# Kernel optimization log

Hardware: AMD Instinct MI355X
Metric: run time of the kernel (lower is better)

The kernel has to match this reference:

```python
import jax, jax.numpy as jnp
import numpy as np

EPS = 1e-08


def setup_inputs() -> dict:
    key = jax.random.key(0)
    B, C, T = 4, 512, 32000
    x = jax.random.normal(key, (B, C, T), dtype=jnp.float32)
    weight = jnp.ones((C,), dtype=jnp.float32)
    bias = jnp.zeros((C,), dtype=jnp.float32)
    return {"x": x, "weight": weight, "bias": bias}


def reference(x, weight, bias):
    # Cumulative LayerNorm over (C, 0..t) for each time step t, 3D input (B, C, T).
    # Note: sum_C(cumsum_T(x)) == cumsum_T(sum_C(x)); reduce channels first (cheaper, same math).
    B, C, T = x.shape
    step = jnp.arange(1, T + 1, dtype=x.dtype)            # (T,)
    count = (step * C)[None, None, :]                     # (1,1,T)
    cum_sum = jnp.cumsum(x.sum(axis=1, keepdims=True), axis=-1)          # (B,1,T)
    cum_sum_sq = jnp.cumsum((x * x).sum(axis=1, keepdims=True), axis=-1)  # (B,1,T)
    cum_mean = cum_sum / count
    cum_var = jnp.maximum(cum_sum_sq / count - cum_mean * cum_mean, 0.0)
    y = (x - cum_mean) / jnp.sqrt(cum_var + EPS)
    return y * weight[None, :, None] + bias[None, :, None]
```

## Files before the change

### kernel.cpp

```cpp
#include <hip/hip_runtime.h>
#include <math.h>

#define EPS 1e-8

constexpr int CSPLIT = 16;
constexpr int CH = 1024;

__global__ __launch_bounds__(256) void clnorm_colsum_b(
    const float4* __restrict__ x4, float4* __restrict__ psum4,
    float4* __restrict__ psumsq4, int b, int C, int T4) {
  int t4 = blockIdx.x * 256 + threadIdx.x;
  if (t4 >= T4) return;
  int s = blockIdx.y;
  int cPer = C / CSPLIT;
  const float4* xp = x4 + ((size_t)b * C + (size_t)s * cPer) * (size_t)T4 + t4;
  float4 sum = make_float4(0.f, 0.f, 0.f, 0.f);
  float4 sq = make_float4(0.f, 0.f, 0.f, 0.f);
#pragma unroll 8
  for (int c = 0; c < cPer; ++c) {
    float4 v = xp[(size_t)c * T4];
    sum.x += v.x;
    sum.y += v.y;
    sum.z += v.z;
    sum.w += v.w;
    sq.x = fmaf(v.x, v.x, sq.x);
    sq.y = fmaf(v.y, v.y, sq.y);
    sq.z = fmaf(v.z, v.z, sq.z);
    sq.w = fmaf(v.w, v.w, sq.w);
  }
  size_t o = (size_t)s * T4 + t4;
  psum4[o] = sum;
  psumsq4[o] = sq;
}

__global__ __launch_bounds__(256) void clnorm_chunktot_b(
    const float4* __restrict__ psum4, const float4* __restrict__ psumsq4,
    double* __restrict__ chunkTot, int T4) {
  int ch = blockIdx.x;
  int tid = threadIdx.x;
  int t4 = ch * 256 + tid;
  double ls = 0.0, lq = 0.0;
  if (t4 < T4) {
#pragma unroll
    for (int k = 0; k < CSPLIT; ++k) {
      float4 s4 = psum4[(size_t)k * T4 + t4];
      float4 q4 = psumsq4[(size_t)k * T4 + t4];
      ls += (double)((s4.x + s4.y) + (s4.z + s4.w));
      lq += (double)((q4.x + q4.y) + (q4.z + q4.w));
    }
  }
  __shared__ double sh_s[256];
  __shared__ double sh_q[256];
  sh_s[tid] = ls;
  sh_q[tid] = lq;
  __syncthreads();
  for (int off = 128; off > 0; off >>= 1) {
    if (tid < off) {
      sh_s[tid] += sh_s[tid + off];
      sh_q[tid] += sh_q[tid + off];
    }
    __syncthreads();
  }
  if (tid == 0) {
    chunkTot[(size_t)ch * 2 + 0] = sh_s[0];
    chunkTot[(size_t)ch * 2 + 1] = sh_q[0];
  }
}

__global__ __launch_bounds__(256) void clnorm_scanemit_b(
    const float4* __restrict__ psum4, const float4* __restrict__ psumsq4,
    const double* __restrict__ chunkTot, float* __restrict__ mean,
    float* __restrict__ rstd, int b, int C, int T, int nCh) {
  int ch = blockIdx.x;
  int tid = threadIdx.x;
  int T4 = T / 4;
  int t4 = ch * 256 + tid;

  __shared__ double tp_s[256];
  __shared__ double tp_q[256];
  __shared__ double off_sq[2];

  if (tid == 0) {
    double os = 0.0, oq = 0.0;
    for (int c0 = 0; c0 < ch; ++c0) {
      os += chunkTot[(size_t)c0 * 2 + 0];
      oq += chunkTot[(size_t)c0 * 2 + 1];
    }
    off_sq[0] = os;
    off_sq[1] = oq;
  }

  double ds[4] = {0.0, 0.0, 0.0, 0.0};
  double dq[4] = {0.0, 0.0, 0.0, 0.0};
  if (t4 < T4) {
#pragma unroll
    for (int k = 0; k < CSPLIT; ++k) {
      float4 s4 = psum4[(size_t)k * T4 + t4];
      float4 q4 = psumsq4[(size_t)k * T4 + t4];
      ds[0] += (double)s4.x;
      ds[1] += (double)s4.y;
      ds[2] += (double)s4.z;
      ds[3] += (double)s4.w;
      dq[0] += (double)q4.x;
      dq[1] += (double)q4.y;
      dq[2] += (double)q4.z;
      dq[3] += (double)q4.w;
    }
  }
  double ts = (ds[0] + ds[1]) + (ds[2] + ds[3]);
  double tq = (dq[0] + dq[1]) + (dq[2] + dq[3]);
  tp_s[tid] = ts;
  tp_q[tid] = tq;
  __syncthreads();
  for (int off = 1; off < 256; off <<= 1) {
    double vs = (tid >= off) ? tp_s[tid - off] : 0.0;
    double vq = (tid >= off) ? tp_q[tid - off] : 0.0;
    __syncthreads();
    tp_s[tid] += vs;
    tp_q[tid] += vq;
    __syncthreads();
  }
  double run_s = off_sq[0] + tp_s[tid] - ts;
  double run_q = off_sq[1] + tp_q[tid] - tq;

  int t0 = t4 * 4;
  float m_out[4], r_out[4];
#pragma unroll
  for (int j = 0; j < 4; ++j) {
    run_s += ds[j];
    run_q += dq[j];
    double cnt = (double)(t0 + j + 1) * (double)C;
    double m = run_s / cnt;
    double var = run_q / cnt - m * m;
    if (var < 0.0) var = 0.0;
    m_out[j] = (float)m;
    r_out[j] = (float)(1.0 / sqrt(var + EPS));
  }
  if (t0 < T) {
    size_t mo = (size_t)b * T + t0;
    *(float4*)(mean + mo) = make_float4(m_out[0], m_out[1], m_out[2], m_out[3]);
    *(float4*)(rstd + mo) = make_float4(r_out[0], r_out[1], r_out[2], r_out[3]);
  }
}

__global__ __launch_bounds__(256) void clnorm_apply_b(
    const float4* __restrict__ x4, const float* __restrict__ w,
    const float* __restrict__ bias, const float4* __restrict__ mean4,
    const float4* __restrict__ rstd4, float4* __restrict__ y4,
    int b, int C, int T4) {
  int t4 = blockIdx.x * 256 + threadIdx.x;
  if (t4 >= T4) return;
  int c = blockIdx.y;
  size_t id = ((size_t)b * C + c) * (size_t)T4 + t4;
  size_t mo = (size_t)b * T4 + t4;
  float4 xv = x4[id];
  float4 mv = mean4[mo];
  float4 rv = rstd4[mo];
  float wc = w[c];
  float bc = bias[c];
  float4 yv;
  yv.x = (xv.x - mv.x) * rv.x * wc + bc;
  yv.y = (xv.y - mv.y) * rv.y * wc + bc;
  yv.z = (xv.z - mv.z) * rv.z * wc + bc;
  yv.w = (xv.w - mv.w) * rv.w * wc + bc;
  y4[id] = yv;
}

extern "C" void kernel_launch(void* const* d_in, const int* in_sizes, int n_in,
                              void* d_out, int out_size, void* d_ws,
                              size_t ws_size, hipStream_t stream) {
  const float* x = (const float*)d_in[0];
  const float* w = (const float*)d_in[1];
  const float* bias = (const float*)d_in[2];
  float* out = (float*)d_out;

  const int B = 4;
  int C = in_sizes[1];
  int T = in_sizes[0] / (B * C);
  int T4 = T / 4;
  int nCh = (T + CH - 1) / CH;

  float* ws = (float*)d_ws;
  size_t pn = (size_t)CSPLIT * T;
  float* psum = ws;
  float* psumsq = psum + pn;
  float* mean = psumsq + pn;
  float* rstd = mean + (size_t)B * T;
  double* chunkTot = (double*)(rstd + (size_t)B * T);

  dim3 gc((T4 + 255) / 256, CSPLIT);
  dim3 g2(nCh);
  dim3 ga((T4 + 255) / 256, C);

  for (int b = 0; b < B; ++b) {
    clnorm_colsum_b<<<gc, 256, 0, stream>>>((const float4*)x, (float4*)psum,
                                            (float4*)psumsq, b, C, T4);
    clnorm_chunktot_b<<<g2, 256, 0, stream>>>((const float4*)psum,
                                              (const float4*)psumsq, chunkTot,
                                              T4);
    clnorm_scanemit_b<<<g2, 256, 0, stream>>>((const float4*)psum,
                                              (const float4*)psumsq, chunkTot,
                                              mean, rstd, b, C, T, nCh);
    clnorm_apply_b<<<ga, 256, 0, stream>>>((const float4*)x, w, bias,
                                           (const float4*)mean,
                                           (const float4*)rstd, (float4*)out,
                                           b, C, T4);
  }
}
```

Before: 529.9 us.

## Fuse cumulative layernorm into single-pass kernel with decoupled look-back scan

```diff
diff --git a/kernel.cpp b/kernel.cpp
--- a/kernel.cpp
+++ b/kernel.cpp
@@ -3,167 +3,207 @@
 
 #define EPS 1e-8
 
-constexpr int CSPLIT = 16;
-constexpr int CH = 1024;
-
-__global__ __launch_bounds__(256) void clnorm_colsum_b(
-    const float4* __restrict__ x4, float4* __restrict__ psum4,
-    float4* __restrict__ psumsq4, int b, int C, int T4) {
-  int t4 = blockIdx.x * 256 + threadIdx.x;
-  if (t4 >= T4) return;
-  int s = blockIdx.y;
-  int cPer = C / CSPLIT;
-  const float4* xp = x4 + ((size_t)b * C + (size_t)s * cPer) * (size_t)T4 + t4;
-  float4 sum = make_float4(0.f, 0.f, 0.f, 0.f);
-  float4 sq = make_float4(0.f, 0.f, 0.f, 0.f);
+constexpr int W = 32;
+constexpr int W4 = W / 4;
+constexpr int NTHR = 512;
+constexpr int PARTS = NTHR / W;
+constexpr int CMAX = 512;
+
+__device__ inline unsigned long long ld_acq(const unsigned long long* p) {
+  return __hip_atomic_load(p, __ATOMIC_ACQUIRE, __HIP_MEMORY_SCOPE_AGENT);
+}
+__device__ inline unsigned long long ld_rlx(const unsigned long long* p) {
+  return __hip_atomic_load(p, __ATOMIC_RELAXED, __HIP_MEMORY_SCOPE_AGENT);
+}
+__device__ inline void st_rlx(unsigned long long* p, unsigned long long v) {
+  __hip_atomic_store(p, v, __ATOMIC_RELAXED, __HIP_MEMORY_SCOPE_AGENT);
+}
+__device__ inline void st_rel(unsigned long long* p, unsigned long long v) {
+  __hip_atomic_store(p, v, __ATOMIC_RELEASE, __HIP_MEMORY_SCOPE_AGENT);
+}
+__device__ inline double u2d(unsigned long long u) {
+  return __builtin_bit_cast(double, u);
+}
+__device__ inline unsigned long long d2u(double d) {
+  return __builtin_bit_cast(unsigned long long, d);
+}
+
+__global__ __launch_bounds__(NTHR, 4) void clnorm_fused(
+    const float4* __restrict__ x4, const float* __restrict__ wgt,
+    const float* __restrict__ bias, float4* __restrict__ y4,
+    unsigned long long* __restrict__ ws_u64, int B, int C, int T, int nCh) {
+  const int T4 = T >> 2;
+  const int tid = threadIdx.x;
+
+  __shared__ float x_sh[CMAX * W];
+  __shared__ float ps_sh[PARTS * W];
+  __shared__ float pq_sh[PARTS * W];
+  __shared__ float w_sh[CMAX];
+  __shared__ float b_sh[CMAX];
+  __shared__ __align__(16) float m_sh[W];
+  __shared__ __align__(16) float r_sh[W];
+  __shared__ int sh_tile;
+
+  unsigned long long* counter = ws_u64;
+  unsigned long long* slots = ws_u64 + 8;
+
+  if (tid == 0)
+    sh_tile = (int)__hip_atomic_fetch_add(counter, 1ull, __ATOMIC_RELAXED,
+                                          __HIP_MEMORY_SCOPE_AGENT);
+  __syncthreads();
+  const int tile = sh_tile;
+  const int b = tile / nCh;
+  const int chunk = tile - b * nCh;
+  const int t0 = chunk * W;
+  const int t40 = t0 >> 2;
+
+  const int nF4 = C * W4;
+#pragma unroll 4
+  for (int f = tid; f < nF4; f += NTHR) {
+    int c = f >> 3;
+    int t4 = f & (W4 - 1);
+    float4 v = make_float4(0.f, 0.f, 0.f, 0.f);
+    if (t40 + t4 < T4) v = x4[(size_t)(b * C + c) * T4 + t40 + t4];
+    *(float4*)&x_sh[c * W + t4 * 4] = v;
+  }
+  for (int c = tid; c < C; c += NTHR) {
+    w_sh[c] = wgt[c];
+    b_sh[c] = bias[c];
+  }
+  __syncthreads();
+
+  {
+    int t = tid & (W - 1);
+    int part = tid >> 5;
+    int cPer = C / PARTS;
+    int c0 = part * cPer;
+    float s = 0.f, q = 0.f;
 #pragma unroll 8
-  for (int c = 0; c < cPer; ++c) {
-    float4 v = xp[(size_t)c * T4];
-    sum.x += v.x;
-    sum.y += v.y;
-    sum.z += v.z;
-    sum.w += v.w;
-    sq.x = fmaf(v.x, v.x, sq.x);
-    sq.y = fmaf(v.y, v.y, sq.y);
-    sq.z = fmaf(v.z, v.z, sq.z);
-    sq.w = fmaf(v.w, v.w, sq.w);
-  }
-  size_t o = (size_t)s * T4 + t4;
-  psum4[o] = sum;
-  psumsq4[o] = sq;
-}
-
-__global__ __launch_bounds__(256) void clnorm_chunktot_b(
-    const float4* __restrict__ psum4, const float4* __restrict__ psumsq4,
-    double* __restrict__ chunkTot, int T4) {
-  int ch = blockIdx.x;
-  int tid = threadIdx.x;
-  int t4 = ch * 256 + tid;
-  double ls = 0.0, lq = 0.0;
-  if (t4 < T4) {
+    for (int k = 0; k < cPer; ++k) {
+      float v = x_sh[(c0 + k) * W + t];
+      s += v;
+      q = fmaf(v, v, q);
+    }
+    ps_sh[part * W + t] = s;
+    pq_sh[part * W + t] = q;
+  }
+  __syncthreads();
+
+  if (tid < 64) {
+    const int lane = tid;
+    double p_s = 0.0, p_q = 0.0;
+    if (lane < W) {
 #pragma unroll
-    for (int k = 0; k < CSPLIT; ++k) {
-      float4 s4 = psum4[(size_t)k * T4 + t4];
-      float4 q4 = psumsq4[(size_t)k * T4 + t4];
-      ls += (double)((s4.x + s4.y) + (s4.z + s4.w));
-      lq += (double)((q4.x + q4.y) + (q4.z + q4.w));
-    }
-  }
-  __shared__ double sh_s[256];
-  __shared__ double sh_q[256];
-  sh_s[tid] = ls;
-  sh_q[tid] = lq;
-  __syncthreads();
-  for (int off = 128; off > 0; off >>= 1) {
-    if (tid < off) {
-      sh_s[tid] += sh_s[tid + off];
-      sh_q[tid] += sh_q[tid + off];
-    }
-    __syncthreads();
-  }
-  if (tid == 0) {
-    chunkTot[(size_t)ch * 2 + 0] = sh_s[0];
-    chunkTot[(size_t)ch * 2 + 1] = sh_q[0];
-  }
-}
-
-__global__ __launch_bounds__(256) void clnorm_scanemit_b(
-    const float4* __restrict__ psum4, const float4* __restrict__ psumsq4,
-    const double* __restrict__ chunkTot, float* __restrict__ mean,
-    float* __restrict__ rstd, int b, int C, int T, int nCh) {
-  int ch = blockIdx.x;
-  int tid = threadIdx.x;
-  int T4 = T / 4;
-  int t4 = ch * 256 + tid;
-
-  __shared__ double tp_s[256];
-  __shared__ double tp_q[256];
-  __shared__ double off_sq[2];
-
-  if (tid == 0) {
-    double os = 0.0, oq = 0.0;
-    for (int c0 = 0; c0 < ch; ++c0) {
-      os += chunkTot[(size_t)c0 * 2 + 0];
-      oq += chunkTot[(size_t)c0 * 2 + 1];
-    }
-    off_sq[0] = os;
-    off_sq[1] = oq;
-  }
-
-  double ds[4] = {0.0, 0.0, 0.0, 0.0};
-  double dq[4] = {0.0, 0.0, 0.0, 0.0};
-  if (t4 < T4) {
-#pragma unroll
-    for (int k = 0; k < CSPLIT; ++k) {
-      float4 s4 = psum4[(size_t)k * T4 + t4];
-      float4 q4 = psumsq4[(size_t)k * T4 + t4];
-      ds[0] += (double)s4.x;
-      ds[1] += (double)s4.y;
-      ds[2] += (double)s4.z;
-      ds[3] += (double)s4.w;
-      dq[0] += (double)q4.x;
-      dq[1] += (double)q4.y;
-      dq[2] += (double)q4.z;
-      dq[3] += (double)q4.w;
-    }
-  }
-  double ts = (ds[0] + ds[1]) + (ds[2] + ds[3]);
-  double tq = (dq[0] + dq[1]) + (dq[2] + dq[3]);
-  tp_s[tid] = ts;
-  tp_q[tid] = tq;
-  __syncthreads();
-  for (int off = 1; off < 256; off <<= 1) {
-    double vs = (tid >= off) ? tp_s[tid - off] : 0.0;
-    double vq = (tid >= off) ? tp_q[tid - off] : 0.0;
-    __syncthreads();
-    tp_s[tid] += vs;
-    tp_q[tid] += vq;
-    __syncthreads();
-  }
-  double run_s = off_sq[0] + tp_s[tid] - ts;
-  double run_q = off_sq[1] + tp_q[tid] - tq;
-
-  int t0 = t4 * 4;
-  float m_out[4], r_out[4];
-#pragma unroll
-  for (int j = 0; j < 4; ++j) {
-    run_s += ds[j];
-    run_q += dq[j];
-    double cnt = (double)(t0 + j + 1) * (double)C;
-    double m = run_s / cnt;
-    double var = run_q / cnt - m * m;
-    if (var < 0.0) var = 0.0;
-    m_out[j] = (float)m;
-    r_out[j] = (float)(1.0 / sqrt(var + EPS));
-  }
-  if (t0 < T) {
-    size_t mo = (size_t)b * T + t0;
-    *(float4*)(mean + mo) = make_float4(m_out[0], m_out[1], m_out[2], m_out[3]);
-    *(float4*)(rstd + mo) = make_float4(r_out[0], r_out[1], r_out[2], r_out[3]);
-  }
-}
-
-__global__ __launch_bounds__(256) void clnorm_apply_b(
-    const float4* __restrict__ x4, const float* __restrict__ w,
-    const float* __restrict__ bias, const float4* __restrict__ mean4,
-    const float4* __restrict__ rstd4, float4* __restrict__ y4,
-    int b, int C, int T4) {
-  int t4 = blockIdx.x * 256 + threadIdx.x;
-  if (t4 >= T4) return;
-  int c = blockIdx.y;
-  size_t id = ((size_t)b * C + c) * (size_t)T4 + t4;
-  size_t mo = (size_t)b * T4 + t4;
-  float4 xv = x4[id];
-  float4 mv = mean4[mo];
-  float4 rv = rstd4[mo];
-  float wc = w[c];
-  float bc = bias[c];
-  float4 yv;
-  yv.x = (xv.x - mv.x) * rv.x * wc + bc;
-  yv.y = (xv.y - mv.y) * rv.y * wc + bc;
-  yv.z = (xv.z - mv.z) * rv.z * wc + bc;
-  yv.w = (xv.w - mv.w) * rv.w * wc + bc;
-  y4[id] = yv;
+      for (int p = 0; p < PARTS; ++p) {
+        p_s += (double)ps_sh[p * W + lane];
+        p_q += (double)pq_sh[p * W + lane];
+      }
+    }
+    for (int off = 1; off < W; off <<= 1) {
+      double vs = __shfl_up(p_s, off, 64);
+      double vq = __shfl_up(p_q, off, 64);
+      if (lane >= off && lane < W) {
+        p_s += vs;
+        p_q += vq;
+      }
+    }
+    double A_s = __shfl(p_s, W - 1, 64);
+    double A_q = __shfl(p_q, W - 1, 64);
+
+    unsigned long long* mySlot = slots + (size_t)tile * 8;
+    if (chunk == 0) {
+      if (lane == 0) {
+        st_rlx(mySlot + 3, d2u(A_s));
+        st_rlx(mySlot + 4, d2u(A_q));
+        st_rel(mySlot + 0, 2ull);
+      }
+    } else if (lane == 0) {
+      st_rlx(mySlot + 1, d2u(A_s));
+      st_rlx(mySlot + 2, d2u(A_q));
+      st_rel(mySlot + 0, 1ull);
+    }
+
+    double E_s = 0.0, E_q = 0.0;
+    if (chunk > 0) {
+      unsigned long long* chain = slots + (size_t)b * nCh * 8;
+      int pos = chunk;
+      while (true) {
+        int idx = pos - 1 - lane;
+        const unsigned long long* ps = chain + (size_t)(idx < 0 ? 0 : idx) * 8;
+        unsigned long long st = 0;
+        if (idx >= 0) st = ld_acq(ps);
+        unsigned long long b2 = __ballot(st == 2ull);
+        unsigned long long b0 = __ballot(st == 0ull);
+        bool got = false;
+        bool full = false;
+        double vs = 0.0, vq = 0.0;
+        if (b2 != 0) {
+          int l2 = __ffsll(b2) - 1;
+          if ((b0 & ((1ull << l2) - 1ull)) == 0) {
+            if (lane < l2) {
+              vs = u2d(ld_rlx(ps + 1));
+              vq = u2d(ld_rlx(ps + 2));
+            } else if (lane == l2) {
+              vs = u2d(ld_rlx(ps + 3));
+              vq = u2d(ld_rlx(ps + 4));
+            }
+            got = true;
+          }
+        } else if (b0 == 0) {
+          vs = u2d(ld_rlx(ps + 1));
+          vq = u2d(ld_rlx(ps + 2));
+          full = true;
+        }
+        if (got || full) {
+          for (int o = 32; o > 0; o >>= 1) {
+            vs += __shfl_down(vs, o, 64);
+            vq += __shfl_down(vq, o, 64);
+          }
+          vs = __shfl(vs, 0, 64);
+          vq = __shfl(vq, 0, 64);
+          E_s += vs;
+          E_q += vq;
+          if (got) break;
+          pos -= 64;
+        } else {
+          __builtin_amdgcn_s_sleep(2);
+        }
+      }
+      if (lane == 0) {
+        st_rlx(mySlot + 3, d2u(E_s + A_s));
+        st_rlx(mySlot + 4, d2u(E_q + A_q));
+        st_rel(mySlot + 0, 2ull);
+      }
+    }
+
+    if (lane < W) {
+      int tg = t0 + lane;
+      double cnt = (double)(tg + 1) * (double)C;
+      double m = (E_s + p_s) / cnt;
+      double var = (E_q + p_q) / cnt - m * m;
+      if (var < 0.0) var = 0.0;
+      m_sh[lane] = (float)m;
+      r_sh[lane] = (float)(1.0 / sqrt(var + EPS));
+    }
+  }
+  __syncthreads();
+
+#pragma unroll 4
+  for (int f = tid; f < nF4; f += NTHR) {
+    int c = f >> 3;
+    int t4 = f & (W4 - 1);
+    if (t40 + t4 >= T4) continue;
+    float4 xv = *(const float4*)&x_sh[c * W + t4 * 4];
+    float4 mv = *(const float4*)&m_sh[t4 * 4];
+    float4 rv = *(const float4*)&r_sh[t4 * 4];
+    float wc = w_sh[c], bc = b_sh[c];
+    float4 yv;
+    yv.x = (xv.x - mv.x) * rv.x * wc + bc;
+    yv.y = (xv.y - mv.y) * rv.y * wc + bc;
+    yv.z = (xv.z - mv.z) * rv.z * wc + bc;
+    yv.w = (xv.w - mv.w) * rv.w * wc + bc;
+    y4[(size_t)(b * C + c) * T4 + t40 + t4] = yv;
+  }
 }
 
 extern "C" void kernel_launch(void* const* d_in, const int* in_sizes, int n_in,
@@ -177,33 +217,13 @@
   const int B = 4;
   int C = in_sizes[1];
   int T = in_sizes[0] / (B * C);
-  int T4 = T / 4;
-  int nCh = (T + CH - 1) / CH;
-
-  float* ws = (float*)d_ws;
-  size_t pn = (size_t)CSPLIT * T;
-  float* psum = ws;
-  float* psumsq = psum + pn;
-  float* mean = psumsq + pn;
-  float* rstd = mean + (size_t)B * T;
-  double* chunkTot = (double*)(rstd + (size_t)B * T);
-
-  dim3 gc((T4 + 255) / 256, CSPLIT);
-  dim3 g2(nCh);
-  dim3 ga((T4 + 255) / 256, C);
-
-  for (int b = 0; b < B; ++b) {
-    clnorm_colsum_b<<<gc, 256, 0, stream>>>((const float4*)x, (float4*)psum,
-                                            (float4*)psumsq, b, C, T4);
-    clnorm_chunktot_b<<<g2, 256, 0, stream>>>((const float4*)psum,
-                                              (const float4*)psumsq, chunkTot,
-                                              T4);
-    clnorm_scanemit_b<<<g2, 256, 0, stream>>>((const float4*)psum,
-                                              (const float4*)psumsq, chunkTot,
-                                              mean, rstd, b, C, T, nCh);
-    clnorm_apply_b<<<ga, 256, 0, stream>>>((const float4*)x, w, bias,
-                                           (const float4*)mean,
-                                           (const float4*)rstd, (float4*)out,
-                                           b, C, T4);
-  }
-}
+  int nCh = (T + W - 1) / W;
+  int nTiles = B * nCh;
+
+  size_t ctrlBytes = 64 + (size_t)nTiles * 64;
+  hipMemsetAsync(d_ws, 0, ctrlBytes, stream);
+
+  clnorm_fused<<<dim3(nTiles), NTHR, 0, stream>>>(
+      (const float4*)x, w, bias, (float4*)out, (unsigned long long*)d_ws, B, C,
+      T, nCh);
+}
```

Result: slower. 818.5 us (+54.5%).
